# Optimization experiments

Hardware: AMD Instinct MI355X
Metric: run time of the kernel (lower is better)

## Reference

```python
import jax, jax.numpy as jnp
import numpy as np
import math

B, H, L, D = 2, 16, 2048, 128


def setup_inputs() -> dict:
    key = jax.random.key(0)
    kq, kk, kv, km, kp = jax.random.split(key, 5)
    q = jax.random.normal(kq, (B, H, L, D), dtype=jnp.float32)
    k = jax.random.normal(kk, (B, H, L, D), dtype=jnp.float32)
    v = jax.random.normal(kv, (B, H, L, D), dtype=jnp.float32)
    mask = jax.random.randint(km, (B, 1, L, L), 0, 2, dtype=jnp.int32)
    probs = jax.random.uniform(kp, (B, L, L), dtype=jnp.float32)
    alpha = jnp.ones((), dtype=jnp.float32)  # learned scalar Parameter, init 1.0
    return {"q": q, "k": k, "v": v, "mask": mask, "probs": probs, "alpha": alpha}


def reference(q, k, v, mask, probs, alpha):
    # scores: (B, H, L, L)
    scale = 1.0 / math.sqrt(q.shape[-1])
    attn_score = jnp.einsum("bhqd,bhkd->bhqk", q, k) * scale
    # additive learned-scale probability bias, broadcast over heads
    attn_score = attn_score + probs[:, None, :, :] * alpha
    # masked_fill(mask == 0, -inf)
    attn_score = jnp.where(mask == 0, -jnp.inf, attn_score)
    attn_p = jax.nn.softmax(attn_score, axis=-1)
    # dropout p=0.0 -> identity
    attention = jnp.einsum("bhqk,bhkd->bhqd", attn_p, v)
    return attention, attn_p
```

## Files before the change

### kernel.cpp

```cpp
#include <hip/hip_runtime.h>

constexpr int BB = 2, HH = 16, LL = 2048, DD = 128;
constexpr int QB = 64, KB = 32, NKT = LL / KB;
constexpr float SCALE = 0.08838834764831845f;

typedef __attribute__((ext_vector_type(8))) short bf16x8;
typedef __attribute__((ext_vector_type(8))) unsigned short u16x8;
typedef __attribute__((ext_vector_type(4))) float f32x4;
typedef __attribute__((ext_vector_type(4))) int i32x4;

static __device__ __forceinline__ unsigned short f2bf(float f) {
  unsigned int u = __builtin_bit_cast(unsigned int, f);
  u += 0x7fffu + ((u >> 16) & 1u);
  return (unsigned short)(u >> 16);
}
static __device__ __forceinline__ float bf2f(unsigned short h) {
  return __builtin_bit_cast(float, (unsigned int)h << 16);
}

#define GLD16(gsrc, ldst) __builtin_amdgcn_global_load_lds( \
    (const __attribute__((address_space(1))) void*)(gsrc), \
    (__attribute__((address_space(3))) void*)(ldst), 16, 0, 0)

__global__ __launch_bounds__(256)
void prep_kernel(const float* __restrict__ k, const float* __restrict__ v,
                 const int* __restrict__ mask, const float* __restrict__ probs,
                 const float* __restrict__ alphap,
                 unsigned short* __restrict__ kbT, unsigned short* __restrict__ vtT,
                 unsigned short* __restrict__ cpw)
{
  __shared__ unsigned short sT[128 * 40];
  const int bid = blockIdx.x;
  const int bh = bid >> 6, kt = bid & 63;
  const int t = threadIdx.x;
  const float alpha = alphap[0];
  const size_t tileBase = (size_t)bid * 4096;
  const float* kg = k + ((size_t)bh * LL + kt * 32) * DD;
  const float* vg = v + ((size_t)bh * LL + kt * 32) * DD;

  #pragma unroll
  for (int s = t; s < 512; s += 256) {
    int dsl = s >> 5, key = s & 31;
    const float* src = kg + key * DD + dsl * 8;
    float4 a = *(const float4*)src;
    float4 c = *(const float4*)(src + 4);
    u16x8 w;
    w[0] = f2bf(a.x); w[1] = f2bf(a.y); w[2] = f2bf(a.z); w[3] = f2bf(a.w);
    w[4] = f2bf(c.x); w[5] = f2bf(c.y); w[6] = f2bf(c.z); w[7] = f2bf(c.w);
    *(u16x8*)(kbT + tileBase + (size_t)s * 8) = w;
  }
  #pragma unroll
  for (int i = 0; i < 4; ++i) {
    int idx = i * 256 + t;
    int key = idx >> 5, d4 = (idx & 31) * 4;
    float4 x = ((const float4*)vg)[idx];
    sT[(d4 + 0) * 40 + key] = f2bf(x.x);
    sT[(d4 + 1) * 40 + key] = f2bf(x.y);
    sT[(d4 + 2) * 40 + key] = f2bf(x.z);
    sT[(d4 + 3) * 40 + key] = f2bf(x.w);
  }
  {
    const float4* ps = (const float4*)probs;
    const int4* ms = (const int4*)mask;
    ushort4* cs = (ushort4*)cpw;
    size_t base = (size_t)bid * 1024;
    #pragma unroll
    for (int i = 0; i < 4; ++i) {
      size_t idx = base + i * 256 + t;
      float4 p = ps[idx];
      int4 m = ms[idx];
      ushort4 o;
      o.x = f2bf(m.x ? p.x * alpha : -1e30f);
      o.y = f2bf(m.y ? p.y * alpha : -1e30f);
      o.z = f2bf(m.z ? p.z * alpha : -1e30f);
      o.w = f2bf(m.w ? p.w * alpha : -1e30f);
      cs[idx] = o;
    }
  }
  __syncthreads();
  #pragma unroll
  for (int s = t; s < 512; s += 256) {
    int kc = s >> 7, d = s & 127;
    u16x8 w = *(const u16x8*)&sT[d * 40 + kc * 8];
    *(u16x8*)(vtT + tileBase + (size_t)s * 8) = w;
  }
}

__global__ __launch_bounds__(256, 6)
void passA_kernel(const float* __restrict__ q, const unsigned short* __restrict__ kbT,
                  const unsigned short* __restrict__ cpw, float* __restrict__ invW)
{
  __shared__ unsigned short sK[2][4096];

  const int tid = threadIdx.x;
  const int lane = tid & 63;
  const int wid = tid >> 6;
  const int l15 = lane & 15;
  const int l4 = lane >> 4;

  const int bid = blockIdx.x;
  const int work = ((bid & 7) << 7) | (bid >> 3);
  const int bh = work >> 5;
  const int qt = work & 31;
  const int b = bh >> 4;
  const int q0 = qt * QB;
  const int row16 = wid << 4;

  const unsigned short* kbh = kbT + (size_t)bh * 64 * 4096;
  const unsigned short* cgrow = cpw + (size_t)b * LL * LL + (size_t)(q0 + row16 + l15) * LL;

  bf16x8 qf0, qf1, qf2, qf3;
  {
    const float* qs = q + (size_t)(bh * LL + q0 + row16 + l15) * DD + l4 * 8;
    #define LQ(FR, KC) { \
      float4 a = *(const float4*)(qs + (KC) * 32); \
      float4 c = *(const float4*)(qs + (KC) * 32 + 4); \
      FR[0]=(short)f2bf(a.x); FR[1]=(short)f2bf(a.y); FR[2]=(short)f2bf(a.z); FR[3]=(short)f2bf(a.w); \
      FR[4]=(short)f2bf(c.x); FR[5]=(short)f2bf(c.y); FR[6]=(short)f2bf(c.z); FR[7]=(short)f2bf(c.w); }
    LQ(qf0, 0) LQ(qf1, 1) LQ(qf2, 2) LQ(qf3, 3)
    #undef LQ
  }

  #define DMA_K(BUF, KT) do { \
    GLD16(kbh + (size_t)(KT) * 4096 + tid * 8,         &sK[BUF][wid << 9]); \
    GLD16(kbh + (size_t)(KT) * 4096 + (256 + tid) * 8, &sK[BUF][2048 + (wid << 9)]); } while (0)

  #define QKS(KC, QF) { \
    bf16x8 k0 = *(const bf16x8*)&sK[cur][(((KC) * 4 + l4) * 32 + l15) * 8]; \
    a0 = __builtin_amdgcn_mfma_f32_16x16x32_bf16(k0, QF, a0, 0, 0, 0); \
    bf16x8 k1 = *(const bf16x8*)&sK[cur][(((KC) * 4 + l4) * 32 + 16 + l15) * 8]; \
    a1 = __builtin_amdgcn_mfma_f32_16x16x32_bf16(k1, QF, a1, 0, 0, 0); }

  DMA_K(0, 0);
  ushort4 cn0 = *(const ushort4*)(cgrow + (l4 << 2));
  ushort4 cn1 = *(const ushort4*)(cgrow + 16 + (l4 << 2));
  float sum = 0.f;
  for (int kt = 0; kt < NKT; ++kt) {
    const int cur = kt & 1;
    __syncthreads();
    if (kt + 1 < NKT) DMA_K(cur ^ 1, kt + 1);
    ushort4 b0 = cn0, b1 = cn1;
    if (kt + 1 < NKT) {
      cn0 = *(const ushort4*)(cgrow + (kt + 1) * 32 + (l4 << 2));
      cn1 = *(const ushort4*)(cgrow + (kt + 1) * 32 + 16 + (l4 << 2));
    }
    f32x4 a0 = {0.f,0.f,0.f,0.f}, a1 = {0.f,0.f,0.f,0.f};
    QKS(0, qf0) QKS(1, qf1) QKS(2, qf2) QKS(3, qf3)
    sum += __expf(a0[0] * SCALE + bf2f(b0.x));
    sum += __expf(a0[1] * SCALE + bf2f(b0.y));
    sum += __expf(a0[2] * SCALE + bf2f(b0.z));
    sum += __expf(a0[3] * SCALE + bf2f(b0.w));
    sum += __expf(a1[0] * SCALE + bf2f(b1.x));
    sum += __expf(a1[1] * SCALE + bf2f(b1.y));
    sum += __expf(a1[2] * SCALE + bf2f(b1.z));
    sum += __expf(a1[3] * SCALE + bf2f(b1.w));
  }
  sum += __shfl_xor(sum, 16, 64);
  sum += __shfl_xor(sum, 32, 64);
  if (l4 == 0)
    invW[(size_t)bh * LL + q0 + row16 + l15] = 1.0f / sum;
  #undef DMA_K
  #undef QKS
}

__global__ __launch_bounds__(256, 4)
void passB_kernel(const float* __restrict__ q, const unsigned short* __restrict__ kbT,
                  const unsigned short* __restrict__ vtT, const unsigned short* __restrict__ cpw,
                  const float* __restrict__ invW,
                  float* __restrict__ outA, float* __restrict__ outP)
{
  __shared__ unsigned short sK[2][4096];
  __shared__ unsigned short sVt[2][4096];

  const int tid = threadIdx.x;
  const int lane = tid & 63;
  const int wid = tid >> 6;
  const int l15 = lane & 15;
  const int l4 = lane >> 4;

  const int bid = blockIdx.x;
  const int work = ((bid & 7) << 7) | (bid >> 3);
  const int bh = work >> 5;
  const int qt = work & 31;
  const int b = bh >> 4;
  const int q0 = qt * QB;
  const int row16 = wid << 4;

  const unsigned short* kbh = kbT + (size_t)bh * 64 * 4096;
  const unsigned short* vbh = vtT + (size_t)bh * 64 * 4096;
  const unsigned short* cgrow = cpw + (size_t)b * LL * LL + (size_t)(q0 + row16 + l15) * LL;
  float* oA = outA + (size_t)(bh * LL + q0) * DD;
  float* oPr = outP + (size_t)bh * LL * LL + (size_t)(q0 + row16 + l15) * LL;

  const float inv = invW[(size_t)bh * LL + q0 + row16 + l15];

  bf16x8 qf0, qf1, qf2, qf3;
  {
    const float* qs = q + (size_t)(bh * LL + q0 + row16 + l15) * DD + l4 * 8;
    #define LQ(FR, KC) { \
      float4 a = *(const float4*)(qs + (KC) * 32); \
      float4 c = *(const float4*)(qs + (KC) * 32 + 4); \
      FR[0]=(short)f2bf(a.x); FR[1]=(short)f2bf(a.y); FR[2]=(short)f2bf(a.z); FR[3]=(short)f2bf(a.w); \
      FR[4]=(short)f2bf(c.x); FR[5]=(short)f2bf(c.y); FR[6]=(short)f2bf(c.z); FR[7]=(short)f2bf(c.w); }
    LQ(qf0, 0) LQ(qf1, 1) LQ(qf2, 2) LQ(qf3, 3)
    #undef LQ
  }

  #define DMA_K(BUF, KT) do { \
    GLD16(kbh + (size_t)(KT) * 4096 + tid * 8,         &sK[BUF][wid << 9]); \
    GLD16(kbh + (size_t)(KT) * 4096 + (256 + tid) * 8, &sK[BUF][2048 + (wid << 9)]); } while (0)
  #define DMA_V(BUF, KT) do { \
    GLD16(vbh + (size_t)(KT) * 4096 + tid * 8,         &sVt[BUF][wid << 9]); \
    GLD16(vbh + (size_t)(KT) * 4096 + (256 + tid) * 8, &sVt[BUF][2048 + (wid << 9)]); } while (0)

  #define QKS(KC, QF) { \
    bf16x8 k0 = *(const bf16x8*)&sK[cur][(((KC) * 4 + l4) * 32 + l15) * 8]; \
    a0 = __builtin_amdgcn_mfma_f32_16x16x32_bf16(k0, QF, a0, 0, 0, 0); \
    bf16x8 k1 = *(const bf16x8*)&sK[cur][(((KC) * 4 + l4) * 32 + 16 + l15) * 8]; \
    a1 = __builtin_amdgcn_mfma_f32_16x16x32_bf16(k1, QF, a1, 0, 0, 0); }

  DMA_K(0, 0); DMA_V(0, 0);
  ushort4 cn0 = *(const ushort4*)(cgrow + (l4 << 2));
  ushort4 cn1 = *(const ushort4*)(cgrow + 16 + (l4 << 2));
  f32x4 oacc[8];
  #pragma unroll
  for (int dt = 0; dt < 8; ++dt) oacc[dt] = (f32x4){0.f,0.f,0.f,0.f};

  const int srcA = l15 + (((l4 << 1) + 0) & 3) * 16;
  const int srcB = l15 + (((l4 << 1) + 1) & 3) * 16;
  const bool hiTile = (l4 >= 2);

  for (int kt = 0; kt < NKT; ++kt) {
    const int cur = kt & 1;
    __syncthreads();
    if (kt + 1 < NKT) { DMA_K(cur ^ 1, kt + 1); DMA_V(cur ^ 1, kt + 1); }
    ushort4 b0 = cn0, b1 = cn1;
    if (kt + 1 < NKT) {
      cn0 = *(const ushort4*)(cgrow + (kt + 1) * 32 + (l4 << 2));
      cn1 = *(const ushort4*)(cgrow + (kt + 1) * 32 + 16 + (l4 << 2));
    }
    f32x4 a0 = {0.f,0.f,0.f,0.f}, a1 = {0.f,0.f,0.f,0.f};
    QKS(0, qf0) QKS(1, qf1) QKS(2, qf2) QKS(3, qf3)

    f32x4 p0, p1;
    p0[0] = __expf(a0[0] * SCALE + bf2f(b0.x)) * inv;
    p0[1] = __expf(a0[1] * SCALE + bf2f(b0.y)) * inv;
    p0[2] = __expf(a0[2] * SCALE + bf2f(b0.z)) * inv;
    p0[3] = __expf(a0[3] * SCALE + bf2f(b0.w)) * inv;
    p1[0] = __expf(a1[0] * SCALE + bf2f(b1.x)) * inv;
    p1[1] = __expf(a1[1] * SCALE + bf2f(b1.y)) * inv;
    p1[2] = __expf(a1[2] * SCALE + bf2f(b1.z)) * inv;
    p1[3] = __expf(a1[3] * SCALE + bf2f(b1.w)) * inv;

    __builtin_nontemporal_store(p0, (f32x4*)(oPr + kt * 32 + (l4 << 2)));
    __builtin_nontemporal_store(p1, (f32x4*)(oPr + kt * 32 + 16 + (l4 << 2)));

    unsigned d00, d01, d10, d11;
    asm("v_cvt_pk_bf16_f32 %0, %1, %2" : "=v"(d00) : "v"(p0[0]), "v"(p0[1]));
    asm("v_cvt_pk_bf16_f32 %0, %1, %2" : "=v"(d01) : "v"(p0[2]), "v"(p0[3]));
    asm("v_cvt_pk_bf16_f32 %0, %1, %2" : "=v"(d10) : "v"(p1[0]), "v"(p1[1]));
    asm("v_cvt_pk_bf16_f32 %0, %1, %2" : "=v"(d11) : "v"(p1[2]), "v"(p1[3]));
    int a00 = __shfl((int)d00, srcA, 64);
    int a01 = __shfl((int)d01, srcA, 64);
    int a02 = __shfl((int)d00, srcB, 64);
    int a03 = __shfl((int)d01, srcB, 64);
    int b00 = __shfl((int)d10, srcA, 64);
    int b01 = __shfl((int)d11, srcA, 64);
    int b02 = __shfl((int)d10, srcB, 64);
    int b03 = __shfl((int)d11, srcB, 64);
    i32x4 fw;
    fw[0] = hiTile ? b00 : a00;
    fw[1] = hiTile ? b01 : a01;
    fw[2] = hiTile ? b02 : a02;
    fw[3] = hiTile ? b03 : a03;
    bf16x8 aP = __builtin_bit_cast(bf16x8, fw);

    #pragma unroll
    for (int dt = 0; dt < 8; ++dt) {
      bf16x8 bV = *(const bf16x8*)&sVt[cur][(l4 * 128 + dt * 16 + l15) * 8];
      oacc[dt] = __builtin_amdgcn_mfma_f32_16x16x32_bf16(aP, bV, oacc[dt], 0, 0, 0);
    }
  }

  #pragma unroll
  for (int dt = 0; dt < 8; ++dt) {
    #pragma unroll
    for (int r = 0; r < 4; ++r) {
      __builtin_nontemporal_store(oacc[dt][r],
          oA + (size_t)(row16 + (l4 << 2) + r) * DD + dt * 16 + l15);
    }
  }
}

extern "C" void kernel_launch(void* const* d_in, const int* in_sizes, int n_in,
                              void* d_out, int out_size, void* d_ws, size_t ws_size,
                              hipStream_t stream) {
  const float* q = (const float*)d_in[0];
  const float* k = (const float*)d_in[1];
  const float* v = (const float*)d_in[2];
  const int* mask = (const int*)d_in[3];
  const float* probs = (const float*)d_in[4];
  const float* alpha = (const float*)d_in[5];
  float* outA = (float*)d_out;
  float* outP = outA + (size_t)BB * HH * LL * DD;
  unsigned short* kbT = (unsigned short*)d_ws;
  unsigned short* vtT = kbT + (size_t)32 * 64 * 4096;
  unsigned short* cpw = vtT + (size_t)32 * 64 * 4096;
  float* invW = (float*)(cpw + (size_t)BB * LL * LL);
  hipLaunchKernelGGL(prep_kernel, dim3(32 * 64), dim3(256), 0, stream,
                     k, v, mask, probs, alpha, kbT, vtT, cpw);
  hipLaunchKernelGGL(passA_kernel, dim3(BB * HH * (LL / QB)), dim3(256), 0, stream,
                     q, kbT, cpw, invW);
  hipLaunchKernelGGL(passB_kernel, dim3(BB * HH * (LL / QB)), dim3(256), 0, stream,
                     q, kbT, vtT, cpw, invW, outA, outP);
}
```

Baseline: 280.3 us.

## Tile-swizzle bias workspace for coalesced loads and use waitcnt-based pipeline in passB

```diff
diff --git a/kernel.cpp b/kernel.cpp
--- a/kernel.cpp
+++ b/kernel.cpp
@@ -27,7 +27,7 @@
                  const int* __restrict__ mask, const float* __restrict__ probs,
                  const float* __restrict__ alphap,
                  unsigned short* __restrict__ kbT, unsigned short* __restrict__ vtT,
-                 unsigned short* __restrict__ cpw)
+                 unsigned short* __restrict__ biasW)
 {
   __shared__ unsigned short sT[128 * 40];
   const int bid = blockIdx.x;
@@ -59,23 +59,31 @@
     sT[(d4 + 2) * 40 + key] = f2bf(x.z);
     sT[(d4 + 3) * 40 + key] = f2bf(x.w);
   }
-  {
-    const float4* ps = (const float4*)probs;
-    const int4* ms = (const int4*)mask;
-    ushort4* cs = (ushort4*)cpw;
-    size_t base = (size_t)bid * 1024;
-    #pragma unroll
-    for (int i = 0; i < 4; ++i) {
-      size_t idx = base + i * 256 + t;
-      float4 p = ps[idx];
-      int4 m = ms[idx];
-      ushort4 o;
-      o.x = f2bf(m.x ? p.x * alpha : -1e30f);
-      o.y = f2bf(m.y ? p.y * alpha : -1e30f);
-      o.z = f2bf(m.z ? p.z * alpha : -1e30f);
-      o.w = f2bf(m.w ? p.w * alpha : -1e30f);
-      cs[idx] = o;
-    }
+  #pragma unroll
+  for (int it = 0; it < 2; ++it) {
+    int tileIdx = bid * 2 + it;
+    int b = tileIdx >> 11;
+    int rem = tileIdx & 2047;
+    int tq = rem >> 6;
+    int tk = rem & 63;
+    int row = ((t >> 6) << 4) + (t & 15);
+    int kc = ((t >> 4) & 3) * 4;
+    const float* pr = probs + (size_t)b * LL * LL + (size_t)(tq * 64 + row) * LL + tk * 32;
+    const int* mr = mask + (size_t)b * LL * LL + (size_t)(tq * 64 + row) * LL + tk * 32;
+    float4 f0 = *(const float4*)(pr + kc);
+    float4 f1 = *(const float4*)(pr + kc + 16);
+    int4 m0 = *(const int4*)(mr + kc);
+    int4 m1 = *(const int4*)(mr + kc + 16);
+    u16x8 o;
+    o[0] = f2bf(m0.x ? f0.x * alpha : -1e30f);
+    o[1] = f2bf(m0.y ? f0.y * alpha : -1e30f);
+    o[2] = f2bf(m0.z ? f0.z * alpha : -1e30f);
+    o[3] = f2bf(m0.w ? f0.w * alpha : -1e30f);
+    o[4] = f2bf(m1.x ? f1.x * alpha : -1e30f);
+    o[5] = f2bf(m1.y ? f1.y * alpha : -1e30f);
+    o[6] = f2bf(m1.z ? f1.z * alpha : -1e30f);
+    o[7] = f2bf(m1.w ? f1.w * alpha : -1e30f);
+    *(u16x8*)(biasW + (size_t)tileIdx * 2048 + t * 8) = o;
   }
   __syncthreads();
   #pragma unroll
@@ -88,7 +96,7 @@
 
 __global__ __launch_bounds__(256, 6)
 void passA_kernel(const float* __restrict__ q, const unsigned short* __restrict__ kbT,
-                  const unsigned short* __restrict__ cpw, float* __restrict__ invW)
+                  const unsigned short* __restrict__ biasW, float* __restrict__ invW)
 {
   __shared__ unsigned short sK[2][4096];
 
@@ -107,7 +115,7 @@
   const int row16 = wid << 4;
 
   const unsigned short* kbh = kbT + (size_t)bh * 64 * 4096;
-  const unsigned short* cgrow = cpw + (size_t)b * LL * LL + (size_t)(q0 + row16 + l15) * LL;
+  const unsigned short* bg = biasW + ((size_t)(b * 32 + qt) * 64) * 2048 + (wid << 9) + (lane << 3);
 
   bf16x8 qf0, qf1, qf2, qf3;
   {
@@ -132,28 +140,24 @@
     a1 = __builtin_amdgcn_mfma_f32_16x16x32_bf16(k1, QF, a1, 0, 0, 0); }
 
   DMA_K(0, 0);
-  ushort4 cn0 = *(const ushort4*)(cgrow + (l4 << 2));
-  ushort4 cn1 = *(const ushort4*)(cgrow + 16 + (l4 << 2));
+  u16x8 cnb = *(const u16x8*)(bg);
   float sum = 0.f;
   for (int kt = 0; kt < NKT; ++kt) {
     const int cur = kt & 1;
     __syncthreads();
     if (kt + 1 < NKT) DMA_K(cur ^ 1, kt + 1);
-    ushort4 b0 = cn0, b1 = cn1;
-    if (kt + 1 < NKT) {
-      cn0 = *(const ushort4*)(cgrow + (kt + 1) * 32 + (l4 << 2));
-      cn1 = *(const ushort4*)(cgrow + (kt + 1) * 32 + 16 + (l4 << 2));
-    }
+    u16x8 bt = cnb;
+    if (kt + 1 < NKT) cnb = *(const u16x8*)(bg + (size_t)(kt + 1) * 2048);
     f32x4 a0 = {0.f,0.f,0.f,0.f}, a1 = {0.f,0.f,0.f,0.f};
     QKS(0, qf0) QKS(1, qf1) QKS(2, qf2) QKS(3, qf3)
-    sum += __expf(a0[0] * SCALE + bf2f(b0.x));
-    sum += __expf(a0[1] * SCALE + bf2f(b0.y));
-    sum += __expf(a0[2] * SCALE + bf2f(b0.z));
-    sum += __expf(a0[3] * SCALE + bf2f(b0.w));
-    sum += __expf(a1[0] * SCALE + bf2f(b1.x));
-    sum += __expf(a1[1] * SCALE + bf2f(b1.y));
-    sum += __expf(a1[2] * SCALE + bf2f(b1.z));
-    sum += __expf(a1[3] * SCALE + bf2f(b1.w));
+    sum += __expf(a0[0] * SCALE + bf2f(bt[0]));
+    sum += __expf(a0[1] * SCALE + bf2f(bt[1]));
+    sum += __expf(a0[2] * SCALE + bf2f(bt[2]));
+    sum += __expf(a0[3] * SCALE + bf2f(bt[3]));
+    sum += __expf(a1[0] * SCALE + bf2f(bt[4]));
+    sum += __expf(a1[1] * SCALE + bf2f(bt[5]));
+    sum += __expf(a1[2] * SCALE + bf2f(bt[6]));
+    sum += __expf(a1[3] * SCALE + bf2f(bt[7]));
   }
   sum += __shfl_xor(sum, 16, 64);
   sum += __shfl_xor(sum, 32, 64);
@@ -165,7 +169,7 @@
 
 __global__ __launch_bounds__(256, 4)
 void passB_kernel(const float* __restrict__ q, const unsigned short* __restrict__ kbT,
-                  const unsigned short* __restrict__ vtT, const unsigned short* __restrict__ cpw,
+                  const unsigned short* __restrict__ vtT, const unsigned short* __restrict__ biasW,
                   const float* __restrict__ invW,
                   float* __restrict__ outA, float* __restrict__ outP)
 {
@@ -188,7 +192,7 @@
 
   const unsigned short* kbh = kbT + (size_t)bh * 64 * 4096;
   const unsigned short* vbh = vtT + (size_t)bh * 64 * 4096;
-  const unsigned short* cgrow = cpw + (size_t)b * LL * LL + (size_t)(q0 + row16 + l15) * LL;
+  const unsigned short* bg = biasW + ((size_t)(b * 32 + qt) * 64) * 2048 + (wid << 9) + (lane << 3);
   float* oA = outA + (size_t)(bh * LL + q0) * DD;
   float* oPr = outP + (size_t)bh * LL * LL + (size_t)(q0 + row16 + l15) * LL;
 
@@ -219,67 +223,71 @@
     bf16x8 k1 = *(const bf16x8*)&sK[cur][(((KC) * 4 + l4) * 32 + 16 + l15) * 8]; \
     a1 = __builtin_amdgcn_mfma_f32_16x16x32_bf16(k1, QF, a1, 0, 0, 0); }
 
-  DMA_K(0, 0); DMA_V(0, 0);
-  ushort4 cn0 = *(const ushort4*)(cgrow + (l4 << 2));
-  ushort4 cn1 = *(const ushort4*)(cgrow + 16 + (l4 << 2));
-  f32x4 oacc[8];
-  #pragma unroll
-  for (int dt = 0; dt < 8; ++dt) oacc[dt] = (f32x4){0.f,0.f,0.f,0.f};
-
   const int srcA = l15 + (((l4 << 1) + 0) & 3) * 16;
   const int srcB = l15 + (((l4 << 1) + 1) & 3) * 16;
   const bool hiTile = (l4 >= 2);
 
-  for (int kt = 0; kt < NKT; ++kt) {
-    const int cur = kt & 1;
-    __syncthreads();
-    if (kt + 1 < NKT) { DMA_K(cur ^ 1, kt + 1); DMA_V(cur ^ 1, kt + 1); }
-    ushort4 b0 = cn0, b1 = cn1;
+  f32x4 oacc[8];
+  #pragma unroll
+  for (int dt = 0; dt < 8; ++dt) oacc[dt] = (f32x4){0.f,0.f,0.f,0.f};
+
+  u16x8 cnb;
+
+  #define BBODY(KT) do { \
+    const int cur = (KT) & 1; \
+    u16x8 bt = cnb; \
+    if ((KT) + 1 < NKT) cnb = *(const u16x8*)(bg + (size_t)((KT) + 1) * 2048); \
+    f32x4 a0 = {0.f,0.f,0.f,0.f}, a1 = {0.f,0.f,0.f,0.f}; \
+    QKS(0, qf0) QKS(1, qf1) QKS(2, qf2) QKS(3, qf3) \
+    f32x4 p0, p1; \
+    p0[0] = __expf(a0[0] * SCALE + bf2f(bt[0])) * inv; \
+    p0[1] = __expf(a0[1] * SCALE + bf2f(bt[1])) * inv; \
+    p0[2] = __expf(a0[2] * SCALE + bf2f(bt[2])) * inv; \
+    p0[3] = __expf(a0[3] * SCALE + bf2f(bt[3])) * inv; \
+    p1[0] = __expf(a1[0] * SCALE + bf2f(bt[4])) * inv; \
+    p1[1] = __expf(a1[1] * SCALE + bf2f(bt[5])) * inv; \
+    p1[2] = __expf(a1[2] * SCALE + bf2f(bt[6])) * inv; \
+    p1[3] = __expf(a1[3] * SCALE + bf2f(bt[7])) * inv; \
+    __builtin_nontemporal_store(p0, (f32x4*)(oPr + (KT) * 32 + (l4 << 2))); \
+    __builtin_nontemporal_store(p1, (f32x4*)(oPr + (KT) * 32 + 16 + (l4 << 2))); \
+    unsigned d00, d01, d10, d11; \
+    asm("v_cvt_pk_bf16_f32 %0, %1, %2" : "=v"(d00) : "v"(p0[0]), "v"(p0[1])); \
+    asm("v_cvt_pk_bf16_f32 %0, %1, %2" : "=v"(d01) : "v"(p0[2]), "v"(p0[3])); \
+    asm("v_cvt_pk_bf16_f32 %0, %1, %2" : "=v"(d10) : "v"(p1[0]), "v"(p1[1])); \
+    asm("v_cvt_pk_bf16_f32 %0, %1, %2" : "=v"(d11) : "v"(p1[2]), "v"(p1[3])); \
+    int a00 = __shfl((int)d00, srcA, 64); \
+    int a01 = __shfl((int)d01, srcA, 64); \
+    int a02 = __shfl((int)d00, srcB, 64); \
+    int a03 = __shfl((int)d01, srcB, 64); \
+    int b00 = __shfl((int)d10, srcA, 64); \
+    int b01 = __shfl((int)d11, srcA, 64); \
+    int b02 = __shfl((int)d10, srcB, 64); \
+    int b03 = __shfl((int)d11, srcB, 64); \
+    i32x4 fw; \
+    fw[0] = hiTile ? b00 : a00; \
+    fw[1] = hiTile ? b01 : a01; \
+    fw[2] = hiTile ? b02 : a02; \
+    fw[3] = hiTile ? b03 : a03; \
+    bf16x8 aP = __builtin_bit_cast(bf16x8, fw); \
+    _Pragma("unroll") \
+    for (int dt = 0; dt < 8; ++dt) { \
+      bf16x8 bV = *(const bf16x8*)&sVt[cur][(l4 * 128 + dt * 16 + l15) * 8]; \
+      oacc[dt] = __builtin_amdgcn_mfma_f32_16x16x32_bf16(aP, bV, oacc[dt], 0, 0, 0); \
+    } \
+  } while (0)
+
+  cnb = *(const u16x8*)(bg);
+  DMA_K(0, 0); DMA_V(0, 0);
+  asm volatile("s_waitcnt vmcnt(0)\n\ts_barrier" ::: "memory");
+  DMA_K(1, 1); DMA_V(1, 1);
+  BBODY(0);
+  for (int kt = 1; kt < NKT; ++kt) {
+    asm volatile("s_waitcnt vmcnt(2)\n\ts_barrier" ::: "memory");
     if (kt + 1 < NKT) {
-      cn0 = *(const ushort4*)(cgrow + (kt + 1) * 32 + (l4 << 2));
-      cn1 = *(const ushort4*)(cgrow + (kt + 1) * 32 + 16 + (l4 << 2));
+      const int c2 = (kt + 1) & 1;
+      DMA_K(c2, kt + 1); DMA_V(c2, kt + 1);
     }
-    f32x4 a0 = {0.f,0.f,0.f,0.f}, a1 = {0.f,0.f,0.f,0.f};
-    QKS(0, qf0) QKS(1, qf1) QKS(2, qf2) QKS(3, qf3)
-
-    f32x4 p0, p1;
-    p0[0] = __expf(a0[0] * SCALE + bf2f(b0.x)) * inv;
-    p0[1] = __expf(a0[1] * SCALE + bf2f(b0.y)) * inv;
-    p0[2] = __expf(a0[2] * SCALE + bf2f(b0.z)) * inv;
-    p0[3] = __expf(a0[3] * SCALE + bf2f(b0.w)) * inv;
-    p1[0] = __expf(a1[0] * SCALE + bf2f(b1.x)) * inv;
-    p1[1] = __expf(a1[1] * SCALE + bf2f(b1.y)) * inv;
-    p1[2] = __expf(a1[2] * SCALE + bf2f(b1.z)) * inv;
-    p1[3] = __expf(a1[3] * SCALE + bf2f(b1.w)) * inv;
-
-    __builtin_nontemporal_store(p0, (f32x4*)(oPr + kt * 32 + (l4 << 2)));
-    __builtin_nontemporal_store(p1, (f32x4*)(oPr + kt * 32 + 16 + (l4 << 2)));
-
-    unsigned d00, d01, d10, d11;
-    asm("v_cvt_pk_bf16_f32 %0, %1, %2" : "=v"(d00) : "v"(p0[0]), "v"(p0[1]));
-    asm("v_cvt_pk_bf16_f32 %0, %1, %2" : "=v"(d01) : "v"(p0[2]), "v"(p0[3]));
-    asm("v_cvt_pk_bf16_f32 %0, %1, %2" : "=v"(d10) : "v"(p1[0]), "v"(p1[1]));
-    asm("v_cvt_pk_bf16_f32 %0, %1, %2" : "=v"(d11) : "v"(p1[2]), "v"(p1[3]));
-    int a00 = __shfl((int)d00, srcA, 64);
-    int a01 = __shfl((int)d01, srcA, 64);
-    int a02 = __shfl((int)d00, srcB, 64);
-    int a03 = __shfl((int)d01, srcB, 64);
-    int b00 = __shfl((int)d10, srcA, 64);
-    int b01 = __shfl((int)d11, srcA, 64);
-    int b02 = __shfl((int)d10, srcB, 64);
-    int b03 = __shfl((int)d11, srcB, 64);
-    i32x4 fw;
-    fw[0] = hiTile ? b00 : a00;
-    fw[1] = hiTile ? b01 : a01;
-    fw[2] = hiTile ? b02 : a02;
-    fw[3] = hiTile ? b03 : a03;
-    bf16x8 aP = __builtin_bit_cast(bf16x8, fw);
-
-    #pragma unroll
-    for (int dt = 0; dt < 8; ++dt) {
-      bf16x8 bV = *(const bf16x8*)&sVt[cur][(l4 * 128 + dt * 16 + l15) * 8];
-      oacc[dt] = __builtin_amdgcn_mfma_f32_16x16x32_bf16(aP, bV, oacc[dt], 0, 0, 0);
-    }
+    BBODY(kt);
   }
 
   #pragma unroll
@@ -305,12 +313,12 @@
   float* outP = outA + (size_t)BB * HH * LL * DD;
   unsigned short* kbT = (unsigned short*)d_ws;
   unsigned short* vtT = kbT + (size_t)32 * 64 * 4096;
-  unsigned short* cpw = vtT + (size_t)32 * 64 * 4096;
-  float* invW = (float*)(cpw + (size_t)BB * LL * LL);
+  unsigned short* biasW = vtT + (size_t)32 * 64 * 4096;
+  float* invW = (float*)(biasW + (size_t)4096 * 2048);
   hipLaunchKernelGGL(prep_kernel, dim3(32 * 64), dim3(256), 0, stream,
-                     k, v, mask, probs, alpha, kbT, vtT, cpw);
+                     k, v, mask, probs, alpha, kbT, vtT, biasW);
   hipLaunchKernelGGL(passA_kernel, dim3(BB * HH * (LL / QB)), dim3(256), 0, stream,
-                     q, kbT, cpw, invW);
+                     q, kbT, biasW, invW);
   hipLaunchKernelGGL(passB_kernel, dim3(BB * HH * (LL / QB)), dim3(256), 0, stream,
-                     q, kbT, vtT, cpw, invW, outA, outP);
-}
+                     q, kbT, vtT, biasW, invW, outA, outP);
+}
```

New measurement: 257.8 us, median of 3. 8.0% less time.
